# Kernel optimization log

Measured on AMD Instinct MI355X. Metric: run time of the kernel, lower is better.

## Reference

```python
import jax, jax.numpy as jnp
import numpy as np


def setup_inputs() -> dict:
    key = jax.random.key(0)
    k1, k2 = jax.random.split(key)
    B, P, H, W = 224, 12, 512, 512  # bands, endmembers, image rows/cols
    E = jax.random.uniform(k1, (1, B, P), dtype=jnp.float32)
    A = jax.random.uniform(k2, (1, P, H, W), dtype=jnp.float32)
    return {"E": E, "A": A}


def reference(E, A):
    # Fan Model (FM) nonlinear mixing.
    # E: (1, B, P) endmember spectra; A: (1, P, H, W) abundances.
    E0 = E[0]          # (B, P)
    A0 = A[0]          # (P, H, W)
    P = E0.shape[-1]

    # Linear mixing: tensordot(E, A[0], dims=([2],[0])) -> (1, B, H, W)
    linear = jnp.einsum('bp,phw->bhw', E0, A0)

    # Pairwise (i<j) bilinear term, vectorized over all endmember pairs.
    mask = jnp.triu(jnp.ones((P, P), dtype=E0.dtype), k=1)        # strict upper triangle
    pairE = (E0[:, :, None] * E0[:, None, :]) * mask               # (B, P, P)
    pairA = A0[:, None, :, :] * A0[None, :, :, :]                  # (P, P, H, W)
    nonlinear = jnp.einsum('bij,ijhw->bhw', pairE, pairA)          # (B, H, W)

    return (linear + nonlinear)[None]  # (1, B, H, W)
```

## Files before the change

kernel.cpp:

```cpp
#include <hip/hip_runtime.h>


#define NP 12
#define NB 224
#define HW (512 * 512)
#define BPG 28
#define NGRP 8
#define BLOCK 256

typedef float vfloat2 __attribute__((ext_vector_type(2)));

__global__ void prep_e2(const float* __restrict__ E, float* __restrict__ E2, int n) {
    int i = blockIdx.x * blockDim.x + threadIdx.x;
    if (i < n) {
        float e = E[i];
        E2[i] = e * e;
    }
}

__global__ __launch_bounds__(BLOCK) void fan_mix(const float* __restrict__ E,
                                                 const float* __restrict__ E2,
                                                 const float* __restrict__ A,
                                                 float* __restrict__ out) {
    const int x2 = blockIdx.x * BLOCK + threadIdx.x;
    const int b0 = blockIdx.y * BPG;

    const vfloat2* __restrict__ A2v = (const vfloat2*)A;
    vfloat2* __restrict__ O2v = (vfloat2*)out;

    vfloat2 a[NP], a2[NP];
#pragma unroll
    for (int p = 0; p < NP; ++p) {
        vfloat2 v = A2v[(size_t)p * (HW / 2) + x2];
        a[p] = v;
        a2[p] = v * v;
    }

#pragma unroll 2
    for (int b = b0; b < b0 + BPG; ++b) {
        float Lx = 0.f, Ly = 0.f, Qx = 0.f, Qy = 0.f;
#pragma unroll
        for (int p = 0; p < NP; ++p) {
            float e = E[b * NP + p];
            float e2 = E2[b * NP + p];
            Lx = fmaf(e, a[p].x, Lx);
            Ly = fmaf(e, a[p].y, Ly);
            Qx = fmaf(e2, a2[p].x, Qx);
            Qy = fmaf(e2, a2[p].y, Qy);
        }
        vfloat2 r;
        r.x = Lx + 0.5f * (Lx * Lx - Qx);
        r.y = Ly + 0.5f * (Ly * Ly - Qy);
        __builtin_nontemporal_store(r, &O2v[(size_t)b * (HW / 2) + x2]);
    }
}

extern "C" void kernel_launch(void* const* d_in, const int* in_sizes, int n_in,
                              void* d_out, int out_size, void* d_ws, size_t ws_size,
                              hipStream_t stream) {
    const float* E = (const float*)d_in[0];
    const float* A = (const float*)d_in[1];
    float* out = (float*)d_out;
    float* E2 = (float*)d_ws;

    prep_e2<<<(NB * NP + 255) / 256, 256, 0, stream>>>(E, E2, NB * NP);

    dim3 grid(HW / (2 * BLOCK), NGRP);
    fan_mix<<<grid, BLOCK, 0, stream>>>(E, E2, A, out);
}
```

Before: 242.5 us.

## Drop E-squared prep kernel and widen fan-mix to float4 per thread

Removes the separate prep kernel that squares E, and computes t=e*a inside the loop so both linear and quadratic sums come from the same product. Each thread now handles four pixels with float4 loads and nontemporal stores, which halves the grid, and the band loop unroll goes from 2 to 4. This drops one kernel launch and the E2 loads, and widens memory transactions. The cost is fewer threads in flight and an extra multiply per term.

```diff
diff --git a/kernel.cpp b/kernel.cpp
--- a/kernel.cpp
+++ b/kernel.cpp
@@ -8,50 +8,35 @@
 #define NGRP 8
 #define BLOCK 256
 
-typedef float vfloat2 __attribute__((ext_vector_type(2)));
-
-__global__ void prep_e2(const float* __restrict__ E, float* __restrict__ E2, int n) {
-    int i = blockIdx.x * blockDim.x + threadIdx.x;
-    if (i < n) {
-        float e = E[i];
-        E2[i] = e * e;
-    }
-}
+typedef float vfloat4 __attribute__((ext_vector_type(4)));
 
 __global__ __launch_bounds__(BLOCK) void fan_mix(const float* __restrict__ E,
-                                                 const float* __restrict__ E2,
                                                  const float* __restrict__ A,
                                                  float* __restrict__ out) {
-    const int x2 = blockIdx.x * BLOCK + threadIdx.x;
+    const int x4 = blockIdx.x * BLOCK + threadIdx.x;
     const int b0 = blockIdx.y * BPG;
 
-    const vfloat2* __restrict__ A2v = (const vfloat2*)A;
-    vfloat2* __restrict__ O2v = (vfloat2*)out;
+    const vfloat4* __restrict__ A4 = (const vfloat4*)A;
+    vfloat4* __restrict__ O4 = (vfloat4*)out;
 
-    vfloat2 a[NP], a2[NP];
+    vfloat4 a[NP];
 #pragma unroll
     for (int p = 0; p < NP; ++p) {
-        vfloat2 v = A2v[(size_t)p * (HW / 2) + x2];
-        a[p] = v;
-        a2[p] = v * v;
+        a[p] = A4[(size_t)p * (HW / 4) + x4];
     }
 
-#pragma unroll 2
+#pragma unroll 4
     for (int b = b0; b < b0 + BPG; ++b) {
-        float Lx = 0.f, Ly = 0.f, Qx = 0.f, Qy = 0.f;
+        vfloat4 L = 0.f, Q = 0.f;
 #pragma unroll
         for (int p = 0; p < NP; ++p) {
             float e = E[b * NP + p];
-            float e2 = E2[b * NP + p];
-            Lx = fmaf(e, a[p].x, Lx);
-            Ly = fmaf(e, a[p].y, Ly);
-            Qx = fmaf(e2, a2[p].x, Qx);
-            Qy = fmaf(e2, a2[p].y, Qy);
+            vfloat4 t = e * a[p];
+            L += t;
+            Q += t * t;
         }
-        vfloat2 r;
-        r.x = Lx + 0.5f * (Lx * Lx - Qx);
-        r.y = Ly + 0.5f * (Ly * Ly - Qy);
-        __builtin_nontemporal_store(r, &O2v[(size_t)b * (HW / 2) + x2]);
+        vfloat4 r = L + 0.5f * (L * L - Q);
+        __builtin_nontemporal_store(r, &O4[(size_t)b * (HW / 4) + x4]);
     }
 }
 
@@ -61,10 +46,7 @@
     const float* E = (const float*)d_in[0];
     const float* A = (const float*)d_in[1];
     float* out = (float*)d_out;
-    float* E2 = (float*)d_ws;
 
-    prep_e2<<<(NB * NP + 255) / 256, 256, 0, stream>>>(E, E2, NB * NP);
-
-    dim3 grid(HW / (2 * BLOCK), NGRP);
-    fan_mix<<<grid, BLOCK, 0, stream>>>(E, E2, A, out);
+    dim3 grid(HW / (4 * BLOCK), NGRP);
+    fan_mix<<<grid, BLOCK, 0, stream>>>(E, A, out);
 }
```

After: 248.3 us. 2.4% more time.
